# Kernel tuning notes

Hardware: AMD Instinct MI355X
Metric: run time of the kernel (lower is better)

Reference implementation:

```python
import jax, jax.numpy as jnp
import numpy as np
from jax import lax

# ---- config (mirrors TrinityGuidance init kwargs) ----
GAMMA = 10.0        # LSE smoothing
M = 64              # RUDY grid size
THRESH = 1.0        # congestion threshold
SIGMA = 1.5         # gaussian smoothing sigma
K_SOFT = 2.0        # soft-bbox sigmoid sharpness
W_WL, W_CONG = 1.0, 0.5

B, V, P, NN, MP = 4, 20000, 400000, 50000, 32

# 4 rotation matrices (0/90/180/270 deg)
R_ALL = jnp.array([[[1, 0], [0, 1]],
                   [[0, -1], [1, 0]],
                   [[-1, 0], [0, -1]],
                   [[0, 1], [-1, 0]]], dtype=jnp.float32)


def _gauss_kernel(sigma):
    ksize = max(int(4 * sigma) | 1, 3)
    x = jnp.arange(ksize, dtype=jnp.float32) - ksize // 2
    g = jnp.exp(-x ** 2 / (2.0 * sigma ** 2))
    g2 = g[None, :] * g[:, None]
    return g2 / g2.sum()  # (k,k)


def setup_inputs() -> dict:
    key = jax.random.key(0)
    ks = jax.random.split(key, 7)
    positions = jax.random.uniform(ks[0], (B, V, 2), minval=-1.0, maxval=1.0)
    pin_to_macro = jax.random.randint(ks[1], (P,), 0, V)
    pin_offsets = jax.random.normal(ks[2], (P, 2)) * 0.01
    n2p = jax.random.randint(ks[3], (NN, MP), 0, P)
    # ragged nets: first cnt pins valid, rest padded with -1 (cnt in [2, MP])
    cnt = jax.random.randint(ks[4], (NN, 1), 2, MP + 1)
    net_to_pin = jnp.where(jnp.arange(MP)[None, :] < cnt, n2p, -1)
    rot_idx = jax.random.randint(ks[5], (B, V), 0, 4)
    rotation_onehot = jax.nn.one_hot(rot_idx, 4, dtype=jnp.float32)
    net_weights = jax.random.uniform(ks[6], (NN,), minval=0.5, maxval=1.5)
    return dict(positions=positions, net_to_pin=net_to_pin,
                pin_to_macro=pin_to_macro, pin_offsets=pin_offsets,
                rotation_onehot=rotation_onehot, net_weights=net_weights)


def _forward(positions, pin_offsets, rotation_onehot, net_weights,
             net_to_pin, pin_to_macro):
    # --- pin positions with rotated offsets ---
    macro_pos = positions[:, pin_to_macro, :]            # (B,P,2) gather
    macro_rot = rotation_onehot[:, pin_to_macro, :]      # (B,P,4)
    Rm = jnp.einsum('bpk,kij->bpij', macro_rot, R_ALL)   # (B,P,2,2)
    rotated = jnp.einsum('bpij,pj->bpi', Rm, pin_offsets)
    pin_pos = macro_pos + rotated                        # (B,P,2)

    valid = net_to_pin >= 0                              # (NN,MP)
    safe = jnp.maximum(net_to_pin, 0)
    net_pin_pos = pin_pos[:, safe, :]                    # (B,NN,MP,2)
    maskf = valid[None, :, :, None]
    masked_max = jnp.where(maskf, net_pin_pos, -1e9)
    masked_min = jnp.where(maskf, net_pin_pos, 1e9)

    # --- WA wirelength via masked double logsumexp per net ---
    gamma = jnp.float32(GAMMA)
    lse_max = jax.nn.logsumexp(gamma * masked_max, axis=2) / gamma   # (B,NN,2)
    lse_min = -jax.nn.logsumexp(-gamma * masked_min, axis=2) / gamma
    wl_per_net = (lse_max - lse_min).sum(-1)             # (B,NN)
    hpwl = (wl_per_net * net_weights[None, :]).sum(1)    # (B,)

    # --- RUDY congestion (separable soft-bbox, no (B,N,M,M) materialization) ---
    bbox_max = masked_max.max(axis=2)                    # (B,NN,2)
    bbox_min = masked_min.min(axis=2)
    bmax = (bbox_max + 1.0) * 0.5 * (M - 1)
    bmin = (bbox_min + 1.0) * 0.5 * (M - 1)
    x_min, y_min = bmin[..., 0:1], bmin[..., 1:2]        # (B,NN,1)
    x_max, y_max = bmax[..., 0:1], bmax[..., 1:2]
    g = jnp.arange(M, dtype=jnp.float32)[None, None, :]  # (1,1,M)
    in_x = jax.nn.sigmoid(K_SOFT * (g - x_min + 0.5)) * \
           jax.nn.sigmoid(K_SOFT * (x_max - g + 0.5))    # (B,NN,M)
    in_y = jax.nn.sigmoid(K_SOFT * (g - y_min + 0.5)) * \
           jax.nn.sigmoid(K_SOFT * (y_max - g + 0.5))    # (B,NN,M)
    bbox_size = jnp.maximum((x_max - x_min + 1.0) * (y_max - y_min + 1.0), 1.0)
    # rudy[b,i,j] = sum_n in_y[b,n,i] * in_x[b,n,j] / bbox_size[b,n]
    rudy = jnp.einsum('bni,bnj->bij', in_y / bbox_size, in_x)
    rudy = rudy[:, None, :, :]                           # (B,1,M,M)

    kernel = _gauss_kernel(SIGMA)                        # (k,k)
    pad = kernel.shape[-1] // 2
    rudy_smooth = lax.conv_general_dilated(
        rudy, kernel[None, None, :, :],
        window_strides=(1, 1), padding=[(pad, pad), (pad, pad)],
        dimension_numbers=('NCHW', 'OIHW', 'NCHW'))
    overflow = jax.nn.relu(rudy_smooth - THRESH)
    penalty = (overflow ** 2).sum(axis=(1, 2, 3))        # (B,)

    return W_WL * hpwl + W_CONG * penalty                # (B,)


def reference(positions, net_to_pin, pin_to_macro, pin_offsets,
              rotation_onehot, net_weights):
    return _forward(positions, pin_offsets, rotation_onehot, net_weights,
                    net_to_pin, pin_to_macro)
```

## Files before the change

### kernel.cpp

```cpp
#include <hip/hip_runtime.h>
#include <cstddef>

namespace {

constexpr int B = 4, V = 20000, P = 400000, NN = 50000, MP = 32;
constexpr float GAMMA = 10.0f, INV_GAMMA = 0.1f;
constexpr float KSOFT = 2.0f;
constexpr float THRESH = 1.0f;
constexpr float W_WL = 1.0f, W_CONG = 0.5f;
constexpr int BPB = 128;
constexpr int NET_GRID = BPB * B;
constexpr int GRPS = 7;
constexpr int NPW = GRPS * 16;
constexpr int A_SUBS = 196;
constexpr int A_GRID = A_SUBS * B;

typedef __attribute__((ext_vector_type(8)))  short bf16x8;
typedef __attribute__((ext_vector_type(16))) float f32x16;

__device__ __forceinline__ float fast_rcp(float x) { return __builtin_amdgcn_rcpf(x); }
__device__ __forceinline__ short f2bf(float f) {
    unsigned u = __float_as_uint(f);
    u += 0x7fffu + ((u >> 16) & 1u);
    return (short)(u >> 16);
}
template <int CTRL>
__device__ __forceinline__ float dpp_mov(float x, float id) {
    return __int_as_float(__builtin_amdgcn_update_dpp(
        __float_as_int(id), __float_as_int(x), CTRL, 0xf, 0xf, false));
}
__device__ __forceinline__ float rdlane(float x, int l) {
    return __int_as_float(__builtin_amdgcn_readlane(__float_as_int(x), l));
}
#define DPP5(x, OP, ID)                              \
    x = OP(x, dpp_mov<0x111>(x, ID));                \
    x = OP(x, dpp_mov<0x112>(x, ID));                \
    x = OP(x, dpp_mov<0x114>(x, ID));                \
    x = OP(x, dpp_mov<0x118>(x, ID));                \
    x = OP(x, dpp_mov<0x142>(x, ID));
__device__ __forceinline__ float op_add(float a, float b) { return a + b; }

__global__ void zero_ws_kernel(float* __restrict__ p, int n) {
    int i = blockIdx.x * blockDim.x + threadIdx.x;
    if (i < n) p[i] = 0.0f;
}

__global__ void macro_prep_kernel(const float* __restrict__ positions,
                                  const float* __restrict__ rot_onehot,
                                  float4* __restrict__ mac) {
    int i = blockIdx.x * blockDim.x + threadIdx.x;
    if (i >= B * V) return;
    float2 pos = ((const float2*)positions)[i];
    float4 w = ((const float4*)rot_onehot)[i];
    mac[i] = make_float4(pos.x, pos.y, w.x - w.z, w.y - w.w);
}

__global__ void pin_pos_kernel(const float4* __restrict__ mac,
                               const int* __restrict__ pin_to_macro,
                               const float* __restrict__ pin_offsets,
                               float* __restrict__ pin_pos) {
    int idx = blockIdx.x * blockDim.x + threadIdx.x;
    if (idx >= B * P) return;
    int b = idx / P;
    int p = idx - b * P;
    int m = pin_to_macro[p];
    float2 off = ((const float2*)pin_offsets)[p];
    float4 md = mac[(size_t)b * V + m];
    ((float2*)pin_pos)[idx] = make_float2(md.x + md.z * off.x - md.w * off.y,
                                          md.y + md.w * off.x + md.z * off.y);
}

__global__ void transpose_n2p_kernel(const int* __restrict__ n2p,
                                     int* __restrict__ n2pT) {
    int i = blockIdx.x * blockDim.x + threadIdx.x;
    if (i >= NN * MP) return;
    int n = i >> 5, j = i & 31;
    n2pT[j * NN + n] = n2p[i];
}

__global__ void __launch_bounds__(256)
bbox_kernel(const float* __restrict__ pin_pos,
            const int* __restrict__ n2pT,
            const float* __restrict__ net_weights,
            float4* __restrict__ bbox,
            float* __restrict__ hpwl) {
    __shared__ float hps[4];
    int blk = blockIdx.x;
    int xcd = blk & 7;
    int b = xcd >> 1;
    int sub = ((blk >> 3) << 1) | (xcd & 1);
    int tid = threadIdx.x;
    int wave = tid >> 6;
    int lane = tid & 63;

    int n = sub * 256 + wave * 64 + lane;
    bool inrange = n < NN;
    int nc = inrange ? n : (NN - 1);

    const float2* pp = (const float2*)(pin_pos + (size_t)b * P * 2);

    int pi[MP];
    #pragma unroll
    for (int j = 0; j < MP; ++j) pi[j] = n2pT[j * NN + nc];

    float ex1 = 0.f, ex2 = 0.f, ey1 = 0.f, ey2 = 0.f;
    float vxmax = -1e30f, vxmin = 1e30f, vymax = -1e30f, vymin = 1e30f;
    #pragma unroll 8
    for (int j = 0; j < MP; ++j) {
        bool v = pi[j] >= 0;
        float2 q = pp[v ? pi[j] : 0];
        float e1x = __expf(GAMMA * q.x);
        float e1y = __expf(GAMMA * q.y);
        ex1 += v ? e1x : 0.f;
        ex2 += v ? fast_rcp(e1x) : 0.f;
        ey1 += v ? e1y : 0.f;
        ey2 += v ? fast_rcp(e1y) : 0.f;
        vxmax = fmaxf(vxmax, v ? q.x : -1e30f);
        vxmin = fminf(vxmin, v ? q.x :  1e30f);
        vymax = fmaxf(vymax, v ? q.y : -1e30f);
        vymin = fminf(vymin, v ? q.y :  1e30f);
    }
    float w = net_weights[nc];
    float wl = __logf(ex1 * ex2 * ey1 * ey2) * INV_GAMMA;
    float hp = inrange ? wl * w : 0.f;

    if (inrange) {
        bbox[(size_t)b * NN + n] = make_float4(
            (vxmin + 1.0f) * 31.5f, (vxmax + 1.0f) * 31.5f,
            (vymin + 1.0f) * 31.5f, (vymax + 1.0f) * 31.5f);
    }
    DPP5(hp, op_add, 0.0f);
    float tot = rdlane(hp, 31) + rdlane(hp, 63);
    if (lane == 0) hps[wave] = tot;
    __syncthreads();
    if (tid == 0) atomicAdd(&hpwl[b], hps[0] + hps[1] + hps[2] + hps[3]);
}

__global__ void __launch_bounds__(256)
rudy_kernel(const float4* __restrict__ bbox,
            float* __restrict__ slabs) {
    __shared__ float lds4[4][4096];
    int x = blockIdx.x;
    int xcd = x & 7;
    int b = xcd >> 1;
    int sub = ((x >> 3) << 1) | (xcd & 1);
    int tid = threadIdx.x;
    int wave = tid >> 6;
    int lane = tid & 63;

    int s = sub * 4 + wave;
    int s0 = s * NPW;
    const float* bbf = (const float*)(bbox + (size_t)b * NN);

    #pragma unroll
    for (int k = 0; k < 7; ++k) {
        int d = s0 * 4 + k * 64 + lane;
        stagewr:
        lds4[wave][k * 64 + lane] = bbf[d < NN * 4 ? d : 0];
    }
    const float4* st = (const float4*)lds4[wave];

    f32x16 acc00, acc01, acc10, acc11;
    #pragma unroll
    for (int r = 0; r < 16; ++r) { acc00[r] = 0.f; acc01[r] = 0.f; acc10[r] = 0.f; acc11[r] = 0.f; }

    int half8 = (lane >> 5) * 8;
    float g2 = (float)(lane & 31);

    float En0 = __expf(fmaf(-KSOFT, g2,  32.0f * KSOFT));
    float Ep0 = __expf(fmaf( KSOFT, g2, -32.0f * KSOFT));
    float EnH = __expf(-KSOFT * g2);
    float EpH = __expf( KSOFT * g2);

    if (s0 < NN) {
        float4 bbc[8];
        #pragma unroll
        for (int j = 0; j < 8; ++j) bbc[j] = st[half8 + j];
        #pragma unroll
        for (int grp = 0; grp < GRPS; ++grp) {
            float4 bbn[8];
            if (grp + 1 < GRPS) {
                #pragma unroll
                for (int j = 0; j < 8; ++j) bbn[j] = st[(grp + 1) * 16 + half8 + j];
            }
            int nb = s0 + grp * 16 + half8;
            bf16x8 A0, A1, B0, B1;
            #pragma unroll
            for (int j = 0; j < 8; ++j) {
                float4 q = bbc[j];
                float u_x = __expf(fmaf( KSOFT, q.x, -32.5f * KSOFT));
                float w_x = __expf(fmaf(-KSOFT, q.y,  31.5f * KSOFT));
                float u_y = __expf(fmaf( KSOFT, q.z, -32.5f * KSOFT));
                float w_y = __expf(fmaf(-KSOFT, q.w,  31.5f * KSOFT));
                float cx = fmaf(u_x, w_x, 1.0f);
                float cy = fmaf(u_y, w_y, 1.0f);
                float inv = (nb + j < NN)
                    ? fast_rcp(fmaxf((q.y - q.x + 1.0f) * (q.w - q.z + 1.0f), 1.0f))
                    : 0.0f;
                float a0 = fast_rcp(fmaf(En0, u_y, fmaf(Ep0, w_y, cy))) * inv;
                float a1 = fast_rcp(fmaf(EnH, u_y, fmaf(EpH, w_y, cy))) * inv;
                float b0 = fast_rcp(fmaf(En0, u_x, fmaf(Ep0, w_x, cx)));
                float b1 = fast_rcp(fmaf(EnH, u_x, fmaf(EpH, w_x, cx)));
                A0[j] = f2bf(a0); A1[j] = f2bf(a1);
                B0[j] = f2bf(b0); B1[j] = f2bf(b1);
            }
            acc00 = __builtin_amdgcn_mfma_f32_32x32x16_bf16(A0, B0, acc00, 0, 0, 0);
            acc01 = __builtin_amdgcn_mfma_f32_32x32x16_bf16(A0, B1, acc01, 0, 0, 0);
            acc10 = __builtin_amdgcn_mfma_f32_32x32x16_bf16(A1, B0, acc10, 0, 0, 0);
            acc11 = __builtin_amdgcn_mfma_f32_32x32x16_bf16(A1, B1, acc11, 0, 0, 0);
            if (grp + 1 < GRPS) {
                #pragma unroll
                for (int j = 0; j < 8; ++j) bbc[j] = bbn[j];
            }
        }
    }

    int col = lane & 31, rq = lane >> 5;
    float* wt = lds4[wave];
    #pragma unroll
    for (int r = 0; r < 16; ++r) {
        int row = (r & 3) + 8 * (r >> 2) + 4 * rq;
        wt[row * 64 + col]             = acc00[r];
        wt[row * 64 + col + 32]        = acc01[r];
        wt[(row + 32) * 64 + col]      = acc10[r];
        wt[(row + 32) * 64 + col + 32] = acc11[r];
    }
    __syncthreads();
    float* slab = slabs + ((size_t)b * BPB + sub) * 4096;
    for (int k = tid; k < 4096; k += 256)
        slab[k] = (lds4[0][k] + lds4[1][k]) + (lds4[2][k] + lds4[3][k]);
}

__global__ void __launch_bounds__(256)
rudy_reduce_kernel(const float* __restrict__ slabs, float* __restrict__ rudy) {
    int blk = blockIdx.x;
    int xcd = blk & 7;
    int b = xcd >> 1;
    int sub = ((blk >> 3) << 1) | (xcd & 1);
    int c = sub * 256 + threadIdx.x;
    const float* base = slabs + (size_t)b * BPB * 4096 + c;
    float a0 = 0.f, a1 = 0.f, a2 = 0.f, a3 = 0.f;
    #pragma unroll 4
    for (int s = 0; s < BPB; s += 4) {
        a0 += base[(size_t)(s + 0) * 4096];
        a1 += base[(size_t)(s + 1) * 4096];
        a2 += base[(size_t)(s + 2) * 4096];
        a3 += base[(size_t)(s + 3) * 4096];
    }
    rudy[b * 4096 + c] = (a0 + a1) + (a2 + a3);
}

__global__ void conv_penalty_kernel(const float* __restrict__ rudy,
                                    float* __restrict__ pen) {
    int blk = blockIdx.x;
    int b = blk >> 4, chunk = blk & 15;
    int r0 = chunk * 4;
    __shared__ float t2[10][64];
    int tid = threadIdx.x;
    for (int k = tid; k < 640; k += 256) {
        int r = k >> 6, c = k & 63, row = r0 - 3 + r;
        t2[r][c] = (row >= 0 && row < 64) ? rudy[b * 4096 + row * 64 + c] : 0.f;
    }
    __syncthreads();
    float g1[7];
    #pragma unroll
    for (int i = 0; i < 7; ++i) { float t = (float)(i - 3); g1[i] = __expf(-t * t / 4.5f); }
    float s1 = g1[0] + g1[1] + g1[2] + g1[3] + g1[4] + g1[5] + g1[6];
    float inv = fast_rcp(s1 * s1);
    int i = tid >> 6, j = tid & 63;
    float acc = 0.f;
    #pragma unroll
    for (int di = -3; di <= 3; ++di) {
        #pragma unroll
        for (int dj = -3; dj <= 3; ++dj) {
            int jj = j + dj;
            float val = (jj >= 0 && jj < 64) ? t2[i + 3 + di][jj] : 0.f;
            acc += g1[di + 3] * g1[dj + 3] * val;
        }
    }
    acc *= inv;
    float ov = acc - THRESH;
    float p = ov > 0.f ? ov * ov : 0.f;
    DPP5(p, op_add, 0.0f);
    float tot = rdlane(p, 31) + rdlane(p, 63);
    if ((tid & 63) == 0) atomicAdd(&pen[b], tot);
}

__global__ void finalize_kernel(const float* __restrict__ hpwl,
                                const float* __restrict__ pen,
                                float* __restrict__ out) {
    int i = threadIdx.x;
    if (i < B) out[i] = W_WL * hpwl[i] + W_CONG * pen[i];
}

}

extern "C" void kernel_launch(void* const* d_in, const int* in_sizes, int n_in,
                              void* d_out, int out_size, void* d_ws, size_t ws_size,
                              hipStream_t stream) {
    const float* positions    = (const float*)d_in[0];
    const int*   net_to_pin   = (const int*)d_in[1];
    const int*   pin_to_macro = (const int*)d_in[2];
    const float* pin_offsets  = (const float*)d_in[3];
    const float* rot_onehot   = (const float*)d_in[4];
    const float* net_weights  = (const float*)d_in[5];
    float* out = (float*)d_out;

    float*  pin_pos = (float*)d_ws;
    float*  rudy    = pin_pos + (size_t)B * P * 2;
    float*  hpwl    = rudy + (size_t)B * 64 * 64;
    float*  pen     = hpwl + B;
    float4* mac     = (float4*)(pen + B);
    float4* bboxb   = mac + (size_t)B * V;
    int*    n2pT    = (int*)(bboxb + (size_t)B * NN);
    float*  slabs   = pin_pos;

    zero_ws_kernel<<<1, 64, 0, stream>>>(hpwl, 2 * B);
    macro_prep_kernel<<<(B * V + 255) / 256, 256, 0, stream>>>(positions, rot_onehot, mac);
    pin_pos_kernel<<<(B * P + 255) / 256, 256, 0, stream>>>(mac, pin_to_macro, pin_offsets, pin_pos);
    transpose_n2p_kernel<<<(NN * MP + 255) / 256, 256, 0, stream>>>(net_to_pin, n2pT);
    bbox_kernel<<<A_GRID, 256, 0, stream>>>(pin_pos, n2pT, net_weights, bboxb, hpwl);
    rudy_kernel<<<NET_GRID, 256, 0, stream>>>(bboxb, slabs);
    rudy_reduce_kernel<<<64, 256, 0, stream>>>(slabs, rudy);
    conv_penalty_kernel<<<64, 256, 0, stream>>>(rudy, pen);
    finalize_kernel<<<1, 64, 0, stream>>>(hpwl, pen, out);
}
```

Baseline: 165.9 us.

## Fuse prep kernels, vectorize pin positions, prefetch all pin gathers in bbox

Measured after the change: 158.3 us. 4.6% less time.

```diff
diff --git a/kernel.cpp b/kernel.cpp
--- a/kernel.cpp
+++ b/kernel.cpp
@@ -14,6 +14,7 @@
 constexpr int NPW = GRPS * 16;
 constexpr int A_SUBS = 196;
 constexpr int A_GRID = A_SUBS * B;
+constexpr int PREP_N = NN * MP;
 
 typedef __attribute__((ext_vector_type(8)))  short bf16x8;
 typedef __attribute__((ext_vector_type(16))) float f32x16;
@@ -40,42 +41,45 @@
     x = OP(x, dpp_mov<0x142>(x, ID));
 __device__ __forceinline__ float op_add(float a, float b) { return a + b; }
 
-__global__ void zero_ws_kernel(float* __restrict__ p, int n) {
+__global__ void __launch_bounds__(256)
+prep_kernel(const float* __restrict__ positions,
+            const float* __restrict__ rot_onehot,
+            float4* __restrict__ mac,
+            const int* __restrict__ n2p,
+            int* __restrict__ n2pT,
+            float* __restrict__ zacc) {
     int i = blockIdx.x * blockDim.x + threadIdx.x;
-    if (i < n) p[i] = 0.0f;
-}
-
-__global__ void macro_prep_kernel(const float* __restrict__ positions,
-                                  const float* __restrict__ rot_onehot,
-                                  float4* __restrict__ mac) {
-    int i = blockIdx.x * blockDim.x + threadIdx.x;
-    if (i >= B * V) return;
-    float2 pos = ((const float2*)positions)[i];
-    float4 w = ((const float4*)rot_onehot)[i];
-    mac[i] = make_float4(pos.x, pos.y, w.x - w.z, w.y - w.w);
-}
-
-__global__ void pin_pos_kernel(const float4* __restrict__ mac,
-                               const int* __restrict__ pin_to_macro,
-                               const float* __restrict__ pin_offsets,
-                               float* __restrict__ pin_pos) {
+    if (i < 2 * B) zacc[i] = 0.0f;
+    if (i < B * V) {
+        float2 pos = ((const float2*)positions)[i];
+        float4 w = ((const float4*)rot_onehot)[i];
+        mac[i] = make_float4(pos.x, pos.y, w.x - w.z, w.y - w.w);
+    }
+    if (i < PREP_N) {
+        int n = i >> 5, j = i & 31;
+        n2pT[j * NN + n] = n2p[i];
+    }
+}
+
+__global__ void __launch_bounds__(256)
+pin_pos_kernel(const float4* __restrict__ mac,
+               const int* __restrict__ pin_to_macro,
+               const float* __restrict__ pin_offsets,
+               float* __restrict__ pin_pos) {
     int idx = blockIdx.x * blockDim.x + threadIdx.x;
-    if (idx >= B * P) return;
-    int b = idx / P;
-    int p = idx - b * P;
-    int m = pin_to_macro[p];
-    float2 off = ((const float2*)pin_offsets)[p];
-    float4 md = mac[(size_t)b * V + m];
-    ((float2*)pin_pos)[idx] = make_float2(md.x + md.z * off.x - md.w * off.y,
-                                          md.y + md.w * off.x + md.z * off.y);
-}
-
-__global__ void transpose_n2p_kernel(const int* __restrict__ n2p,
-                                     int* __restrict__ n2pT) {
-    int i = blockIdx.x * blockDim.x + threadIdx.x;
-    if (i >= NN * MP) return;
-    int n = i >> 5, j = i & 31;
-    n2pT[j * NN + n] = n2p[i];
+    if (idx >= B * P / 2) return;
+    int b = idx / (P / 2);
+    int t = idx - b * (P / 2);
+    int2 m2 = ((const int2*)pin_to_macro)[t];
+    float4 o2 = ((const float4*)pin_offsets)[t];
+    float4 md0 = mac[(size_t)b * V + m2.x];
+    float4 md1 = mac[(size_t)b * V + m2.y];
+    float4 r;
+    r.x = md0.x + md0.z * o2.x - md0.w * o2.y;
+    r.y = md0.y + md0.w * o2.x + md0.z * o2.y;
+    r.z = md1.x + md1.z * o2.z - md1.w * o2.w;
+    r.w = md1.y + md1.w * o2.z + md1.z * o2.w;
+    ((float4*)pin_pos)[idx] = r;
 }
 
 __global__ void __launch_bounds__(256)
@@ -103,22 +107,25 @@
     #pragma unroll
     for (int j = 0; j < MP; ++j) pi[j] = n2pT[j * NN + nc];
 
+    float2 q[MP];
+    #pragma unroll
+    for (int j = 0; j < MP; ++j) q[j] = pp[pi[j] >= 0 ? pi[j] : 0];
+
     float ex1 = 0.f, ex2 = 0.f, ey1 = 0.f, ey2 = 0.f;
     float vxmax = -1e30f, vxmin = 1e30f, vymax = -1e30f, vymin = 1e30f;
-    #pragma unroll 8
+    #pragma unroll
     for (int j = 0; j < MP; ++j) {
         bool v = pi[j] >= 0;
-        float2 q = pp[v ? pi[j] : 0];
-        float e1x = __expf(GAMMA * q.x);
-        float e1y = __expf(GAMMA * q.y);
+        float e1x = __expf(GAMMA * q[j].x);
+        float e1y = __expf(GAMMA * q[j].y);
         ex1 += v ? e1x : 0.f;
         ex2 += v ? fast_rcp(e1x) : 0.f;
         ey1 += v ? e1y : 0.f;
         ey2 += v ? fast_rcp(e1y) : 0.f;
-        vxmax = fmaxf(vxmax, v ? q.x : -1e30f);
-        vxmin = fminf(vxmin, v ? q.x :  1e30f);
-        vymax = fmaxf(vymax, v ? q.y : -1e30f);
-        vymin = fminf(vymin, v ? q.y :  1e30f);
+        vxmax = fmaxf(vxmax, v ? q[j].x : -1e30f);
+        vxmin = fminf(vxmin, v ? q[j].x :  1e30f);
+        vymax = fmaxf(vymax, v ? q[j].y : -1e30f);
+        vymin = fminf(vymin, v ? q[j].y :  1e30f);
     }
     float w = net_weights[nc];
     float wl = __logf(ex1 * ex2 * ey1 * ey2) * INV_GAMMA;
@@ -155,7 +162,6 @@
     #pragma unroll
     for (int k = 0; k < 7; ++k) {
         int d = s0 * 4 + k * 64 + lane;
-        stagewr:
         lds4[wave][k * 64 + lane] = bbf[d < NN * 4 ? d : 0];
     }
     const float4* st = (const float4*)lds4[wave];
@@ -315,10 +321,10 @@
     int*    n2pT    = (int*)(bboxb + (size_t)B * NN);
     float*  slabs   = pin_pos;
 
-    zero_ws_kernel<<<1, 64, 0, stream>>>(hpwl, 2 * B);
-    macro_prep_kernel<<<(B * V + 255) / 256, 256, 0, stream>>>(positions, rot_onehot, mac);
-    pin_pos_kernel<<<(B * P + 255) / 256, 256, 0, stream>>>(mac, pin_to_macro, pin_offsets, pin_pos);
-    transpose_n2p_kernel<<<(NN * MP + 255) / 256, 256, 0, stream>>>(net_to_pin, n2pT);
+    prep_kernel<<<(PREP_N + 255) / 256, 256, 0, stream>>>(
+        positions, rot_onehot, mac, net_to_pin, n2pT, hpwl);
+    pin_pos_kernel<<<(B * P / 2 + 255) / 256, 256, 0, stream>>>(
+        mac, pin_to_macro, pin_offsets, pin_pos);
     bbox_kernel<<<A_GRID, 256, 0, stream>>>(pin_pos, n2pT, net_weights, bboxb, hpwl);
     rudy_kernel<<<NET_GRID, 256, 0, stream>>>(bboxb, slabs);
     rudy_reduce_kernel<<<64, 256, 0, stream>>>(slabs, rudy);
```
